# Performance work log

Hardware: AMD Instinct MI355X
Metric: run time of the kernel (lower is better)

Reference implementation:

```python
import jax, jax.numpy as jnp
import numpy as np

D_MODEL = 1024
H = 16
D_HEAD = D_MODEL // H
MASK_VAL = -1e30


def setup_inputs() -> dict:
    key = jax.random.key(0)
    ks = jax.random.split(key, 10)
    B, S = 2, 2048
    scale = 1.0 / np.sqrt(D_MODEL)
    return {
        "query": jax.random.normal(ks[0], (B, S, D_MODEL), jnp.float32),
        "key": jax.random.normal(ks[1], (B, S, D_MODEL), jnp.float32),
        "value": jax.random.normal(ks[2], (B, S, D_MODEL), jnp.float32),
        "mask": jax.random.randint(ks[3], (B, S, S), 0, 2) > 0,
        "Wq": jax.random.normal(ks[4], (D_MODEL, D_MODEL), jnp.float32) * scale,
        "bq": jnp.zeros((D_MODEL,), jnp.float32),
        "Wk": jax.random.normal(ks[5], (D_MODEL, D_MODEL), jnp.float32) * scale,
        "bk": jnp.zeros((D_MODEL,), jnp.float32),
        "Wv": jax.random.normal(ks[6], (D_MODEL, D_MODEL), jnp.float32) * scale,
        "bv": jnp.zeros((D_MODEL,), jnp.float32),
    }


def _split_heads(x, B, S):
    # [B,S,D] -> [B,H,S,Dh]
    return x.reshape(B, S, H, D_HEAD).transpose(0, 2, 1, 3)


def reference(query, key, value, mask, Wq, bq, Wk, bk, Wv, bv):
    B, S, _ = query.shape
    q = _split_heads(query @ Wq.T + bq, B, S)
    k = _split_heads(key @ Wk.T + bk, B, S)
    v = _split_heads(value @ Wv.T + bv, B, S)
    # scale by sqrt of per-head dim (query.size(-1) after split)
    q = q / jnp.sqrt(jnp.asarray(D_HEAD, q.dtype))
    scores = jnp.einsum("bhqd,bhkd->bhqk", q, k)
    scores = jnp.where(mask[:, None, :, :], MASK_VAL, scores)
    attn = jax.nn.softmax(scores, axis=-1)
    out = jnp.einsum("bhqk,bhkd->bhqd", attn, v)
    return out.transpose(0, 2, 1, 3).reshape(B, S, D_MODEL)
```

## Files before the change

### kernel.cpp

```cpp
#include <hip/hip_runtime.h>
#include <hip/hip_bf16.h>

#define D_MODEL 1024
#define NH 16
#define DH 64
#define S_LEN 2048
#define BATCH 2
#define NEG_BIG -3e38f
#define QSCALE (0.125f * 1.44269504088896f)

#define KV_HSTRIDE (S_LEN * DH)
#define WS_V_OFF   (NH * KV_HSTRIDE)
#define KVB_WORDS  (2 * NH * KV_HSTRIDE)
#define MB_WORDS   ((S_LEN / 64) * S_LEN)
#define KTILE 128
#define NT (S_LEN / KTILE)
#define X_ELEMS (BATCH * S_LEN * D_MODEL)
#define W_ELEMS (D_MODEL * D_MODEL)
#define KSTR 88

typedef __attribute__((ext_vector_type(8))) short bf16x8;
typedef __attribute__((ext_vector_type(4))) float f32x4;

static __device__ inline unsigned short f2bf(float f) {
    union { float f; unsigned u; } v; v.f = f;
    unsigned r = v.u + 0x7fffu + ((v.u >> 16) & 1u);
    return (unsigned short)(r >> 16);
}
static __device__ inline unsigned cvt2(float a, float b) {
    union { __hip_bfloat162 h2; unsigned u; } cv;
    cv.h2 = __float22bfloat162_rn(make_float2(a, b));
    return cv.u;
}
static __device__ inline bf16x8 pack8(f32x4 a, f32x4 b) {
    union { bf16x8 v; unsigned u[4]; } r;
    r.u[0] = cvt2(a[0], a[1]); r.u[1] = cvt2(a[2], a[3]);
    r.u[2] = cvt2(b[0], b[1]); r.u[3] = cvt2(b[2], b[3]);
    return r.v;
}
static __device__ inline bf16x8 cvt8(const float* __restrict__ p) {
    return pack8(*(const f32x4*)p, *(const f32x4*)(p + 4));
}
static __device__ inline float exp2_fast(float x) {
#if __has_builtin(__builtin_amdgcn_exp2f)
    return __builtin_amdgcn_exp2f(x);
#else
    return exp2f(x);
#endif
}
static __device__ inline void gload_lds16(const unsigned short* __restrict__ g,
                                          unsigned short* l, int lane) {
#if __has_builtin(__builtin_amdgcn_global_load_lds)
    __builtin_amdgcn_global_load_lds(
        (const __attribute__((address_space(1))) void*)g,
        (__attribute__((address_space(3))) void*)l, 16, 0, 0);
#else
    *(bf16x8*)((char*)l + lane * 16) = *(const bf16x8*)g;
#endif
}
static __device__ inline int vperm(int s) {
    return (s & ~31) | ((s & 12) << 1) | ((s & 16) >> 2) | (s & 3);
}

__global__ __launch_bounds__(256) void cvt_kernel(
    const float* __restrict__ q, const float* __restrict__ k,
    const float* __restrict__ v,
    const float* __restrict__ Wq, const float* __restrict__ Wk,
    const float* __restrict__ Wv,
    unsigned short* __restrict__ xb, unsigned short* __restrict__ wb)
{
    const int by = blockIdx.y;
    const float* src;
    unsigned short* dst;
    int t;
    if (blockIdx.x < 1024) {
        src = by == 0 ? q : (by == 1 ? k : v);
        dst = xb + (size_t)by * X_ELEMS;
        t = blockIdx.x * 256 + threadIdx.x;
    } else {
        src = by == 0 ? Wq : (by == 1 ? Wk : Wv);
        dst = wb + (size_t)by * W_ELEMS;
        t = (blockIdx.x - 1024) * 256 + threadIdx.x;
    }
    const size_t o = (size_t)t * 16;
    *(bf16x8*)&dst[o]     = cvt8(src + o);
    *(bf16x8*)&dst[o + 8] = cvt8(src + o + 8);
}

__global__ __launch_bounds__(256) void pack_mask_kernel(
    const int* __restrict__ mask, unsigned long long* __restrict__ mbits,
    int b_base)
{
    const int w    = blockIdx.x * 4 + (threadIdx.x >> 6);
    const int lane = threadIdx.x & 63;
    const int b    = b_base + (w >> 16);
    const int rem  = w & 65535;
    const int kt   = rem >> 11;
    const int s    = rem & 2047;
    const int v = mask[((size_t)b * S_LEN + s) * S_LEN + kt * 64 + lane];
    const unsigned long long bits = __ballot(v != 0);
    if (lane == 0) mbits[w] = bits;
}

__global__ __launch_bounds__(256) void proj_v2_kernel(
    const unsigned short* __restrict__ xb, const unsigned short* __restrict__ wb,
    const float* __restrict__ bq, const float* __restrict__ bk,
    const float* __restrict__ bv,
    float* __restrict__ q_out, unsigned short* __restrict__ ws)
{
    const int bx = blockIdx.x;
    const int by = blockIdx.y;
    const int z  = by >> 3;
    const int c0 = (by & 7) * 128;

    const unsigned short* A  = xb + (size_t)z * X_ELEMS;
    const unsigned short* Bw = wb + (size_t)z * W_ELEMS;
    const float* bias = z == 0 ? bq : (z == 1 ? bk : bv);

    const int tid  = threadIdx.x;
    const int wave = tid >> 6;
    const int lane = tid & 63;
    const int quad = lane >> 4;
    const int l16  = lane & 15;
    const int m0   = (wave & 1) * 64;
    const int n0   = (wave >> 1) * 64;

    __shared__ __align__(16) unsigned short As[128 * 32];
    __shared__ __align__(16) unsigned short Bs[128 * 32];

    const int r_lo = wave * 16 + (lane >> 2);
    const int r_hi = (wave + 4) * 16 + (lane >> 2);
    const int segu = (lane & 3) * 8;
    const int row0 = bx * 128;

    f32x4 acc[4][4] = {};

    for (int kk = 0; kk < D_MODEL; kk += 32) {
        gload_lds16(A  + (size_t)(row0 + r_lo) * D_MODEL + kk + segu, &As[wave * 512], lane);
        gload_lds16(A  + (size_t)(row0 + r_hi) * D_MODEL + kk + segu, &As[(wave + 4) * 512], lane);
        gload_lds16(Bw + (size_t)(c0 + r_lo) * D_MODEL + kk + segu, &Bs[wave * 512], lane);
        gload_lds16(Bw + (size_t)(c0 + r_hi) * D_MODEL + kk + segu, &Bs[(wave + 4) * 512], lane);
        __syncthreads();

        bf16x8 af[4], bfr[4];
#pragma unroll
        for (int i = 0; i < 4; ++i)
            af[i] = *(const bf16x8*)&As[(m0 + i * 16 + l16) * 32 + quad * 8];
#pragma unroll
        for (int j = 0; j < 4; ++j)
            bfr[j] = *(const bf16x8*)&Bs[(n0 + j * 16 + l16) * 32 + quad * 8];
#pragma unroll
        for (int i = 0; i < 4; ++i)
#pragma unroll
            for (int j = 0; j < 4; ++j)
                acc[i][j] = __builtin_amdgcn_mfma_f32_16x16x32_bf16(
                    af[i], bfr[j], acc[i][j], 0, 0, 0);
        __syncthreads();
    }

#pragma unroll
    for (int j = 0; j < 4; ++j) {
        const int cl  = c0 + n0 + j * 16 + l16;
        const float bval = bias[cl];
        const int h  = cl >> 6;
        const int dh = cl & 63;
#pragma unroll
        for (int i = 0; i < 4; ++i) {
#pragma unroll
            for (int r = 0; r < 4; ++r) {
                const int row = row0 + m0 + i * 16 + quad * 4 + r;
                const float v = acc[i][j][r] + bval;
                if (z == 0) {
                    q_out[(size_t)row * D_MODEL + cl] = v * QSCALE;
                } else {
                    unsigned short* slab = ws + (size_t)(row >> 11) * KVB_WORDS;
                    const int s = row & 2047;
                    if (z == 1)
                        slab[(size_t)h * KV_HSTRIDE + s * DH + dh] = f2bf(v);
                    else
                        slab[WS_V_OFF + (size_t)h * KV_HSTRIDE + dh * S_LEN + vperm(s)] = f2bf(v);
                }
            }
        }
    }
}

__global__ __launch_bounds__(256) void proj_fb_kernel(
    const float* __restrict__ q_in, const float* __restrict__ k_in,
    const float* __restrict__ v_in,
    const float* __restrict__ Wq, const float* __restrict__ bq,
    const float* __restrict__ Wk, const float* __restrict__ bk,
    const float* __restrict__ Wv, const float* __restrict__ bv,
    float* __restrict__ q_out, unsigned short* __restrict__ ws, int b_base)
{
    const int bx = blockIdx.x;
    const int by = blockIdx.y;
    const int z  = by >> 3;
    const int c0 = (by & 7) * 128;

    const float* x    = z == 0 ? q_in : (z == 1 ? k_in : v_in);
    const float* W    = z == 0 ? Wq   : (z == 1 ? Wk   : Wv);
    const float* bias = z == 0 ? bq   : (z == 1 ? bk   : bv);

    const int tid  = threadIdx.x;
    const int wave = tid >> 6;
    const int lane = tid & 63;
    const int quad = lane >> 4;
    const int l16  = lane & 15;
    const int m0   = (wave & 1) * 64;
    const int n0   = (wave >> 1) * 64;

    __shared__ __align__(16) unsigned short As[128][40];
    __shared__ __align__(16) unsigned short Bs[128][40];

    const int srow = tid >> 1;
    const int kcol = (tid & 1) * 16;
    const int row0 = b_base * S_LEN + bx * 128;
    const float* ag = x + (size_t)(row0 + srow) * D_MODEL + kcol;
    const float* bg = W + (size_t)(c0 + srow) * D_MODEL + kcol;

    f32x4 acc[4][4] = {};

    for (int kk = 0; kk < D_MODEL; kk += 32) {
        {
            f32x4 a0 = *(const f32x4*)(ag + kk);
            f32x4 a1 = *(const f32x4*)(ag + kk + 4);
            f32x4 a2 = *(const f32x4*)(ag + kk + 8);
            f32x4 a3 = *(const f32x4*)(ag + kk + 12);
            f32x4 b0 = *(const f32x4*)(bg + kk);
            f32x4 b1 = *(const f32x4*)(bg + kk + 4);
            f32x4 b2 = *(const f32x4*)(bg + kk + 8);
            f32x4 b3 = *(const f32x4*)(bg + kk + 12);
            *(bf16x8*)&As[srow][kcol]     = pack8(a0, a1);
            *(bf16x8*)&As[srow][kcol + 8] = pack8(a2, a3);
            *(bf16x8*)&Bs[srow][kcol]     = pack8(b0, b1);
            *(bf16x8*)&Bs[srow][kcol + 8] = pack8(b2, b3);
        }
        __syncthreads();

        bf16x8 af[4], bfr[4];
#pragma unroll
        for (int i = 0; i < 4; ++i)
            af[i] = *(const bf16x8*)&As[m0 + i * 16 + l16][quad * 8];
#pragma unroll
        for (int j = 0; j < 4; ++j)
            bfr[j] = *(const bf16x8*)&Bs[n0 + j * 16 + l16][quad * 8];
#pragma unroll
        for (int i = 0; i < 4; ++i)
#pragma unroll
            for (int j = 0; j < 4; ++j)
                acc[i][j] = __builtin_amdgcn_mfma_f32_16x16x32_bf16(
                    af[i], bfr[j], acc[i][j], 0, 0, 0);
        __syncthreads();
    }

#pragma unroll
    for (int j = 0; j < 4; ++j) {
        const int cl  = c0 + n0 + j * 16 + l16;
        const float bval = bias[cl];
        const int h  = cl >> 6;
        const int dh = cl & 63;
#pragma unroll
        for (int i = 0; i < 4; ++i) {
#pragma unroll
            for (int r = 0; r < 4; ++r) {
                const int row = row0 + m0 + i * 16 + quad * 4 + r;
                const float v = acc[i][j][r] + bval;
                if (z == 0) {
                    q_out[(size_t)row * D_MODEL + cl] = v * QSCALE;
                } else {
                    const int b_rel = (row >> 11) - b_base;
                    const int s     = row & 2047;
                    unsigned short* slab = ws + (size_t)b_rel * KVB_WORDS;
                    if (z == 1)
                        slab[(size_t)h * KV_HSTRIDE + s * DH + dh] = f2bf(v);
                    else
                        slab[WS_V_OFF + (size_t)h * KV_HSTRIDE + dh * S_LEN + vperm(s)] = f2bf(v);
                }
            }
        }
    }
}

__global__ __launch_bounds__(256) void attn_kernel(
    const unsigned short* __restrict__ ws,
    const unsigned long long* __restrict__ mbits,
    const int* __restrict__ mask,
    float* __restrict__ out, int b_base, int use_bits)
{
    const int h     = blockIdx.x;
    const int qtile = blockIdx.y;
    const int bz    = blockIdx.z;
    const int b0    = b_base + bz;

    const unsigned short* K  = ws + (size_t)bz * KVB_WORDS + (size_t)h * KV_HSTRIDE;
    const unsigned short* Vg = K + WS_V_OFF;
    const unsigned long long* mb = mbits + (size_t)bz * MB_WORDS;

    const int tid  = threadIdx.x;
    const int wave = tid >> 6;
    const int lane = tid & 63;
    const int quad = lane >> 4;
    const int l16  = lane & 15;
    const int q0   = qtile * 64;

    __shared__ __align__(16) unsigned short Vt[64][136];
    __shared__ __align__(16) unsigned short Kt[128 * KSTR];

    bf16x8 aq0, aq1;
    {
        const float* qrow =
            out + (size_t)(b0 * S_LEN + q0 + wave * 16 + l16) * D_MODEL + h * DH;
        aq0 = cvt8(qrow + quad * 8);
        aq1 = cvt8(qrow + 32 + quad * 8);
    }

    const int qg = q0 + wave * 16 + l16;
    float l_lane = 0.f;
    f32x4 o_acc[4] = {};

    const int krow = tid >> 1, kc = (tid & 1) * 32;
    const int vrow = tid >> 2, vc = (tid & 3) * 32;
    bf16x8 kr[4], vr[4];
    {
        const unsigned short* kp = K + (size_t)krow * DH + kc;
        const unsigned short* vp = Vg + (size_t)vrow * S_LEN + vc;
#pragma unroll
        for (int i = 0; i < 4; ++i) {
            kr[i] = *(const bf16x8*)(kp + 8 * i);
            vr[i] = *(const bf16x8*)(vp + 8 * i);
        }
    }

    for (int kt = 0; kt < NT; ++kt) {
#pragma unroll
        for (int i = 0; i < 4; ++i) {
            *(bf16x8*)&Kt[krow * KSTR + kc + 8 * i] = kr[i];
            *(bf16x8*)&Vt[vrow][vc + 8 * i]         = vr[i];
        }
        __syncthreads();

        if (kt + 1 < NT) {
            const unsigned short* kp = K + (size_t)((kt + 1) * KTILE + krow) * DH + kc;
            const unsigned short* vp = Vg + (size_t)vrow * S_LEN + (kt + 1) * KTILE + vc;
#pragma unroll
            for (int i = 0; i < 4; ++i) {
                kr[i] = *(const bf16x8*)(kp + 8 * i);
                vr[i] = *(const bf16x8*)(vp + 8 * i);
            }
        }

        unsigned long long wm0 = 0ull, wm1 = 0ull;
        if (use_bits) {
            wm0 = mb[(size_t)(2 * kt) * S_LEN + qg] >> (quad * 4);
            wm1 = mb[(size_t)(2 * kt + 1) * S_LEN + qg] >> (quad * 4);
        }

        f32x4 s[8];
#pragma unroll
        for (int blk = 0; blk < 8; ++blk) {
            const unsigned short* kb = &Kt[(blk * 16 + l16) * KSTR];
            bf16x8 k0 = *(const bf16x8*)&kb[quad * 8];
            bf16x8 k1 = *(const bf16x8*)&kb[32 + quad * 8];
            s[blk] = (f32x4){0.f, 0.f, 0.f, 0.f};
            s[blk] = __builtin_amdgcn_mfma_f32_16x16x32_bf16(k0, aq0, s[blk], 0, 0, 0);
            s[blk] = __builtin_amdgcn_mfma_f32_16x16x32_bf16(k1, aq1, s[blk], 0, 0, 0);
        }

#pragma unroll
        for (int blk = 0; blk < 8; ++blk) {
            const unsigned long long w = (blk < 4) ? wm0 : wm1;
            const int sh = (blk & 3) * 16;
#pragma unroll
            for (int r = 0; r < 4; ++r) {
                bool masked;
                if (use_bits) {
                    masked = (w >> (sh + r)) & 1ull;
                } else {
                    const int kg = kt * KTILE + blk * 16 + quad * 4 + r;
                    masked = mask[((size_t)(b0 * S_LEN) + qg) * S_LEN + kg] != 0;
                }
                const float p = masked ? 0.0f : exp2_fast(s[blk][r]);
                s[blk][r] = p;
                l_lane += p;
            }
        }

        bf16x8 af[4];
#pragma unroll
        for (int c = 0; c < 4; ++c) {
            union { bf16x8 v; unsigned u[4]; } pk;
            pk.u[0] = cvt2(s[2 * c][0],     s[2 * c][1]);
            pk.u[1] = cvt2(s[2 * c][2],     s[2 * c][3]);
            pk.u[2] = cvt2(s[2 * c + 1][0], s[2 * c + 1][1]);
            pk.u[3] = cvt2(s[2 * c + 1][2], s[2 * c + 1][3]);
            af[c] = pk.v;
        }

#pragma unroll
        for (int d = 0; d < 4; ++d) {
#pragma unroll
            for (int c = 0; c < 4; ++c) {
                bf16x8 bv = *(const bf16x8*)&Vt[d * 16 + l16][c * 32 + quad * 8];
                o_acc[d] = __builtin_amdgcn_mfma_f32_16x16x32_bf16(af[c], bv, o_acc[d], 0, 0, 0);
            }
        }
        __syncthreads();
    }

    l_lane += __shfl_xor(l_lane, 16, 64);
    l_lane += __shfl_xor(l_lane, 32, 64);

#pragma unroll
    for (int r = 0; r < 4; ++r) {
        const float lsum = __shfl(l_lane, quad * 4 + r, 64);
        const float inv  = 1.0f / fmaxf(lsum, 1e-30f);
        const int qgr = q0 + wave * 16 + quad * 4 + r;
#pragma unroll
        for (int d = 0; d < 4; ++d)
            out[((size_t)(b0 * S_LEN) + qgr) * D_MODEL + h * DH + d * 16 + l16] =
                o_acc[d][r] * inv;
    }
}

extern "C" void kernel_launch(void* const* d_in, const int* in_sizes, int n_in,
                              void* d_out, int out_size, void* d_ws, size_t ws_size,
                              hipStream_t stream) {
    const float* query = (const float*)d_in[0];
    const float* key   = (const float*)d_in[1];
    const float* value = (const float*)d_in[2];
    const int*   mask  = (const int*)d_in[3];
    const float* Wq    = (const float*)d_in[4];
    const float* bq    = (const float*)d_in[5];
    const float* Wk    = (const float*)d_in[6];
    const float* bk    = (const float*)d_in[7];
    const float* Wv    = (const float*)d_in[8];
    const float* bv    = (const float*)d_in[9];

    unsigned short* ws   = (unsigned short*)d_ws;
    float*          outp = (float*)d_out;

    const size_t KV_BYTES = (size_t)KVB_WORDS * 2;
    const size_t MB_BYTES = (size_t)MB_WORDS * 8;
    const size_t XB_BYTES = (size_t)3 * X_ELEMS * 2;
    const size_t WB_BYTES = (size_t)3 * W_ELEMS * 2;
    const size_t base2    = 2 * KV_BYTES + 2 * MB_BYTES;

    if (ws_size >= base2 + XB_BYTES + WB_BYTES) {
        unsigned long long* mbits = (unsigned long long*)(ws + 2 * KVB_WORDS);
        unsigned short* xb = ws + base2 / 2;
        unsigned short* wb = xb + (size_t)3 * X_ELEMS;
        cvt_kernel<<<dim3(1280, 3), 256, 0, stream>>>(
            query, key, value, Wq, Wk, Wv, xb, wb);
        proj_v2_kernel<<<dim3(32, 24), 256, 0, stream>>>(
            xb, wb, bq, bk, bv, outp, ws);
        pack_mask_kernel<<<dim3(2 * MB_WORDS / 4), 256, 0, stream>>>(mask, mbits, 0);
        attn_kernel<<<dim3(NH, S_LEN / 64, 2), 256, 0, stream>>>(
            ws, mbits, mask, outp, 0, 1);
    } else if (ws_size >= base2) {
        unsigned long long* mbits = (unsigned long long*)(ws + 2 * KVB_WORDS);
        proj_fb_kernel<<<dim3(32, 24), 256, 0, stream>>>(
            query, key, value, Wq, bq, Wk, bk, Wv, bv, outp, ws, 0);
        pack_mask_kernel<<<dim3(2 * MB_WORDS / 4), 256, 0, stream>>>(mask, mbits, 0);
        attn_kernel<<<dim3(NH, S_LEN / 64, 2), 256, 0, stream>>>(
            ws, mbits, mask, outp, 0, 1);
    } else if (ws_size >= KV_BYTES + MB_BYTES) {
        unsigned long long* mbits = (unsigned long long*)(ws + KVB_WORDS);
        for (int b0 = 0; b0 < BATCH; ++b0) {
            proj_fb_kernel<<<dim3(16, 24), 256, 0, stream>>>(
                query, key, value, Wq, bq, Wk, bk, Wv, bv, outp, ws, b0);
            pack_mask_kernel<<<dim3(MB_WORDS / 4), 256, 0, stream>>>(mask, mbits, b0);
            attn_kernel<<<dim3(NH, S_LEN / 64, 1), 256, 0, stream>>>(
                ws, mbits, mask, outp, b0, 1);
        }
    } else {
        for (int b0 = 0; b0 < BATCH; ++b0) {
            proj_fb_kernel<<<dim3(16, 24), 256, 0, stream>>>(
                query, key, value, Wq, bq, Wk, bk, Wv, bv, outp, ws, b0);
            attn_kernel<<<dim3(NH, S_LEN / 64, 1), 256, 0, stream>>>(
                ws, (const unsigned long long*)ws, mask, outp, b0, 0);
        }
    }
}
```

Measured before the change: 274.4 us.

## Process two 64-row query tiles per attention block to reuse staged K/V

Each attention block now handles 128 query rows instead of 64: each wave holds two sets of Q fragments, accumulators and row sums, and reuses the same K and V tiles staged in shared memory for both. The grid's query dimension is halved accordingly. This cuts global K/V traffic and LDS staging per query and adds independent MFMA work for latency hiding. In exchange it raises register pressure, which may lower occupancy, and halves the block count.

```diff
diff --git a/kernel.cpp b/kernel.cpp
--- a/kernel.cpp
+++ b/kernel.cpp
@@ -6,7 +6,6 @@
 #define DH 64
 #define S_LEN 2048
 #define BATCH 2
-#define NEG_BIG -3e38f
 #define QSCALE (0.125f * 1.44269504088896f)
 
 #define KV_HSTRIDE (S_LEN * DH)
@@ -302,22 +301,23 @@
     const int lane = tid & 63;
     const int quad = lane >> 4;
     const int l16  = lane & 15;
-    const int q0   = qtile * 64;
+    const int q0   = qtile * 128;
 
     __shared__ __align__(16) unsigned short Vt[64][136];
     __shared__ __align__(16) unsigned short Kt[128 * KSTR];
 
-    bf16x8 aq0, aq1;
+    bf16x8 aq0a, aq1a, aq0b, aq1b;
     {
-        const float* qrow =
+        const float* qa =
             out + (size_t)(b0 * S_LEN + q0 + wave * 16 + l16) * D_MODEL + h * DH;
-        aq0 = cvt8(qrow + quad * 8);
-        aq1 = cvt8(qrow + 32 + quad * 8);
+        const float* qb = qa + (size_t)64 * D_MODEL;
+        aq0a = cvt8(qa + quad * 8);  aq1a = cvt8(qa + 32 + quad * 8);
+        aq0b = cvt8(qb + quad * 8);  aq1b = cvt8(qb + 32 + quad * 8);
     }
 
     const int qg = q0 + wave * 16 + l16;
-    float l_lane = 0.f;
-    f32x4 o_acc[4] = {};
+    float l_a = 0.f, l_b = 0.f;
+    f32x4 o_a[4] = {}, o_b[4] = {};
 
     const int krow = tid >> 1, kc = (tid & 1) * 32;
     const int vrow = tid >> 2, vc = (tid & 3) * 32;
@@ -350,51 +350,66 @@
             }
         }
 
-        unsigned long long wm0 = 0ull, wm1 = 0ull;
+        unsigned long long wm0a = 0ull, wm1a = 0ull, wm0b = 0ull, wm1b = 0ull;
         if (use_bits) {
-            wm0 = mb[(size_t)(2 * kt) * S_LEN + qg] >> (quad * 4);
-            wm1 = mb[(size_t)(2 * kt + 1) * S_LEN + qg] >> (quad * 4);
-        }
-
-        f32x4 s[8];
-#pragma unroll
-        for (int blk = 0; blk < 8; ++blk) {
-            const unsigned short* kb = &Kt[(blk * 16 + l16) * KSTR];
-            bf16x8 k0 = *(const bf16x8*)&kb[quad * 8];
-            bf16x8 k1 = *(const bf16x8*)&kb[32 + quad * 8];
-            s[blk] = (f32x4){0.f, 0.f, 0.f, 0.f};
-            s[blk] = __builtin_amdgcn_mfma_f32_16x16x32_bf16(k0, aq0, s[blk], 0, 0, 0);
-            s[blk] = __builtin_amdgcn_mfma_f32_16x16x32_bf16(k1, aq1, s[blk], 0, 0, 0);
-        }
-
-#pragma unroll
-        for (int blk = 0; blk < 8; ++blk) {
-            const unsigned long long w = (blk < 4) ? wm0 : wm1;
-            const int sh = (blk & 3) * 16;
-#pragma unroll
-            for (int r = 0; r < 4; ++r) {
-                bool masked;
-                if (use_bits) {
-                    masked = (w >> (sh + r)) & 1ull;
-                } else {
-                    const int kg = kt * KTILE + blk * 16 + quad * 4 + r;
-                    masked = mask[((size_t)(b0 * S_LEN) + qg) * S_LEN + kg] != 0;
+            wm0a = mb[(size_t)(2 * kt) * S_LEN + qg] >> (quad * 4);
+            wm1a = mb[(size_t)(2 * kt + 1) * S_LEN + qg] >> (quad * 4);
+            wm0b = mb[(size_t)(2 * kt) * S_LEN + qg + 64] >> (quad * 4);
+            wm1b = mb[(size_t)(2 * kt + 1) * S_LEN + qg + 64] >> (quad * 4);
+        }
+
+        bf16x8 af_a[4], af_b[4];
+#pragma unroll
+        for (int c = 0; c < 4; ++c) {
+            f32x4 sa[2], sb[2];
+#pragma unroll
+            for (int j = 0; j < 2; ++j) {
+                const int blk = 2 * c + j;
+                const unsigned short* kb = &Kt[(blk * 16 + l16) * KSTR];
+                bf16x8 k0 = *(const bf16x8*)&kb[quad * 8];
+                bf16x8 k1 = *(const bf16x8*)&kb[32 + quad * 8];
+                f32x4 z = {0.f, 0.f, 0.f, 0.f};
+                sa[j] = __builtin_amdgcn_mfma_f32_16x16x32_bf16(k0, aq0a, z, 0, 0, 0);
+                sa[j] = __builtin_amdgcn_mfma_f32_16x16x32_bf16(k1, aq1a, sa[j], 0, 0, 0);
+                sb[j] = __builtin_amdgcn_mfma_f32_16x16x32_bf16(k0, aq0b, z, 0, 0, 0);
+                sb[j] = __builtin_amdgcn_mfma_f32_16x16x32_bf16(k1, aq1b, sb[j], 0, 0, 0);
+            }
+#pragma unroll
+            for (int j = 0; j < 2; ++j) {
+                const int blk = 2 * c + j;
+                const unsigned long long wa = (blk < 4) ? wm0a : wm1a;
+                const unsigned long long wb = (blk < 4) ? wm0b : wm1b;
+                const int sh = (blk & 3) * 16;
+#pragma unroll
+                for (int r = 0; r < 4; ++r) {
+                    bool ma, mbk;
+                    if (use_bits) {
+                        ma  = (wa >> (sh + r)) & 1ull;
+                        mbk = (wb >> (sh + r)) & 1ull;
+                    } else {
+                        const int kg = kt * KTILE + blk * 16 + quad * 4 + r;
+                        ma  = mask[((size_t)(b0 * S_LEN) + qg) * S_LEN + kg] != 0;
+                        mbk = mask[((size_t)(b0 * S_LEN) + qg + 64) * S_LEN + kg] != 0;
+                    }
+                    const float pa = ma  ? 0.0f : exp2_fast(sa[j][r]);
+                    const float pb = mbk ? 0.0f : exp2_fast(sb[j][r]);
+                    sa[j][r] = pa; l_a += pa;
+                    sb[j][r] = pb; l_b += pb;
                 }
-                const float p = masked ? 0.0f : exp2_fast(s[blk][r]);
-                s[blk][r] = p;
-                l_lane += p;
-            }
-        }
-
-        bf16x8 af[4];
-#pragma unroll
-        for (int c = 0; c < 4; ++c) {
-            union { bf16x8 v; unsigned u[4]; } pk;
-            pk.u[0] = cvt2(s[2 * c][0],     s[2 * c][1]);
-            pk.u[1] = cvt2(s[2 * c][2],     s[2 * c][3]);
-            pk.u[2] = cvt2(s[2 * c + 1][0], s[2 * c + 1][1]);
-            pk.u[3] = cvt2(s[2 * c + 1][2], s[2 * c + 1][3]);
-            af[c] = pk.v;
+            }
+            {
+                union { bf16x8 v; unsigned u[4]; } pk;
+                pk.u[0] = cvt2(sa[0][0], sa[0][1]);
+                pk.u[1] = cvt2(sa[0][2], sa[0][3]);
+                pk.u[2] = cvt2(sa[1][0], sa[1][1]);
+                pk.u[3] = cvt2(sa[1][2], sa[1][3]);
+                af_a[c] = pk.v;
+                pk.u[0] = cvt2(sb[0][0], sb[0][1]);
+                pk.u[1] = cvt2(sb[0][2], sb[0][3]);
+                pk.u[2] = cvt2(sb[1][0], sb[1][1]);
+                pk.u[3] = cvt2(sb[1][2], sb[1][3]);
+                af_b[c] = pk.v;
+            }
         }
 
 #pragma unroll
@@ -402,24 +417,32 @@
 #pragma unroll
             for (int c = 0; c < 4; ++c) {
                 bf16x8 bv = *(const bf16x8*)&Vt[d * 16 + l16][c * 32 + quad * 8];
-                o_acc[d] = __builtin_amdgcn_mfma_f32_16x16x32_bf16(af[c], bv, o_acc[d], 0, 0, 0);
+                o_a[d] = __builtin_amdgcn_mfma_f32_16x16x32_bf16(af_a[c], bv, o_a[d], 0, 0, 0);
+                o_b[d] = __builtin_amdgcn_mfma_f32_16x16x32_bf16(af_b[c], bv, o_b[d], 0, 0, 0);
             }
         }
         __syncthreads();
     }
 
-    l_lane += __shfl_xor(l_lane, 16, 64);
-    l_lane += __shfl_xor(l_lane, 32, 64);
+    l_a += __shfl_xor(l_a, 16, 64);
+    l_a += __shfl_xor(l_a, 32, 64);
+    l_b += __shfl_xor(l_b, 16, 64);
+    l_b += __shfl_xor(l_b, 32, 64);
 
 #pragma unroll
     for (int r = 0; r < 4; ++r) {
-        const float lsum = __shfl(l_lane, quad * 4 + r, 64);
-        const float inv  = 1.0f / fmaxf(lsum, 1e-30f);
+        const float la = __shfl(l_a, quad * 4 + r, 64);
+        const float lb = __shfl(l_b, quad * 4 + r, 64);
+        const float ia = 1.0f / fmaxf(la, 1e-30f);
+        const float ib = 1.0f / fmaxf(lb, 1e-30f);
         const int qgr = q0 + wave * 16 + quad * 4 + r;
 #pragma unroll
-        for (int d = 0; d < 4; ++d)
+        for (int d = 0; d < 4; ++d) {
             out[((size_t)(b0 * S_LEN) + qgr) * D_MODEL + h * DH + d * 16 + l16] =
-                o_acc[d][r] * inv;
+                o_a[d][r] * ia;
+            out[((size_t)(b0 * S_LEN) + qgr + 64) * D_MODEL + h * DH + d * 16 + l16] =
+                o_b[d][r] * ib;
+        }
     }
 }
 
@@ -455,14 +478,14 @@
         proj_v2_kernel<<<dim3(32, 24), 256, 0, stream>>>(
             xb, wb, bq, bk, bv, outp, ws);
         pack_mask_kernel<<<dim3(2 * MB_WORDS / 4), 256, 0, stream>>>(mask, mbits, 0);
-        attn_kernel<<<dim3(NH, S_LEN / 64, 2), 256, 0, stream>>>(
+        attn_kernel<<<dim3(NH, S_LEN / 128, 2), 256, 0, stream>>>(
             ws, mbits, mask, outp, 0, 1);
     } else if (ws_size >= base2) {
         unsigned long long* mbits = (unsigned long long*)(ws + 2 * KVB_WORDS);
         proj_fb_kernel<<<dim3(32, 24), 256, 0, stream>>>(
             query, key, value, Wq, bq, Wk, bk, Wv, bv, outp, ws, 0);
         pack_mask_kernel<<<dim3(2 * MB_WORDS / 4), 256, 0, stream>>>(mask, mbits, 0);
-        attn_kernel<<<dim3(NH, S_LEN / 64, 2), 256, 0, stream>>>(
+        attn_kernel<<<dim3(NH, S_LEN / 128, 2), 256, 0, stream>>>(
             ws, mbits, mask, outp, 0, 1);
     } else if (ws_size >= KV_BYTES + MB_BYTES) {
         unsigned long long* mbits = (unsigned long long*)(ws + KVB_WORDS);
@@ -470,14 +493,14 @@
             proj_fb_kernel<<<dim3(16, 24), 256, 0, stream>>>(
                 query, key, value, Wq, bq, Wk, bk, Wv, bv, outp, ws, b0);
             pack_mask_kernel<<<dim3(MB_WORDS / 4), 256, 0, stream>>>(mask, mbits, b0);
-            attn_kernel<<<dim3(NH, S_LEN / 64, 1), 256, 0, stream>>>(
+            attn_kernel<<<dim3(NH, S_LEN / 128, 1), 256, 0, stream>>>(
                 ws, mbits, mask, outp, b0, 1);
         }
     } else {
         for (int b0 = 0; b0 < BATCH; ++b0) {
             proj_fb_kernel<<<dim3(16, 24), 256, 0, stream>>>(
                 query, key, value, Wq, bq, Wk, bk, Wv, bv, outp, ws, b0);
-            attn_kernel<<<dim3(NH, S_LEN / 64, 1), 256, 0, stream>>>(
+            attn_kernel<<<dim3(NH, S_LEN / 128, 1), 256, 0, stream>>>(
                 ws, (const unsigned long long*)ws, mask, outp, b0, 0);
         }
     }
```

Measured after the change: 266.9 us. -2.7%, faster.
